# Kernel optimization log

Measured on AMD Instinct MI355X. Metric: run time of the kernel, lower is better.

The kernel has to match this reference:

```python
import jax, jax.numpy as jnp
import numpy as np

B, T, E, H = 8, 2048, 1024, 1024  # batch, seq, embed, head size

def setup_inputs() -> dict:
    key = jax.random.key(0)
    k1, k2, k3, k4 = jax.random.split(key, 4)
    x = jax.random.normal(k1, (B, T, E), dtype=jnp.float32)
    # torch nn.Linear weights are [out, in]; scale down for stability
    Wk = jax.random.normal(k2, (H, E), dtype=jnp.float32) * (E ** -0.5)
    Wq = jax.random.normal(k3, (H, E), dtype=jnp.float32) * (E ** -0.5)
    Wv = jax.random.normal(k4, (H, E), dtype=jnp.float32) * (E ** -0.5)
    return {"x": x, "Wk": Wk, "Wq": Wq, "Wv": Wv}

def reference(x, Wk, Wq, Wv):
    Bx, Tx, Ex = x.shape
    k = jnp.einsum('bte,he->bth', x, Wk)   # [B,T,H]
    q = jnp.einsum('bte,he->bth', x, Wq)
    v = jnp.einsum('bte,he->bth', x, Wv)
    # NOTE: original scales by embed_dim**-0.5 (z = input last dim), not head size
    scores = jnp.einsum('bth,bsh->bts', q, k) * (Ex ** -0.5)  # [B,T,T]
    causal = jnp.tril(jnp.ones((Tx, Tx), dtype=bool))
    scores = jnp.where(causal, scores, -jnp.inf)
    wei = jax.nn.softmax(scores, axis=-1)
    return jnp.einsum('bts,bsh->bth', wei, v)
```

## Files before the change

kernel.cpp:

```cpp
#include <hip/hip_runtime.h>
#include <hip/hip_bf16.h>

typedef unsigned short u16;
typedef __bf16 bf16x8 __attribute__((ext_vector_type(8)));
typedef unsigned short u16x8 __attribute__((ext_vector_type(8)));
typedef unsigned short u16x4 __attribute__((ext_vector_type(4)));
typedef float f32x4 __attribute__((ext_vector_type(4)));
typedef float f32x16 __attribute__((ext_vector_type(16)));

#define B_ 8
#define T_ 2048
#define E_ 1024
#define H_ 1024
#define M_ (B_ * T_)
#define INF __builtin_inff()

__device__ inline u16 f2bf(float f) {
    __bf16 h = (__bf16)f;
    return __builtin_bit_cast(u16, h);
}
__device__ inline float bf2f(u16 u) {
    unsigned v = (unsigned)u << 16;
    return __builtin_bit_cast(float, v);
}
__device__ inline bf16x8 load_frag(const u16* p) {
    u16x8 u = *(const u16x8*)p;
    return __builtin_bit_cast(bf16x8, u);
}
__device__ inline void gload_lds16(const u16* g, u16* l) {
    __builtin_amdgcn_global_load_lds(
        (__attribute__((address_space(1))) unsigned int*)(g),
        (__attribute__((address_space(3))) unsigned int*)(l), 16, 0, 0);
}

__global__ void castk(const float* __restrict__ in, u16* __restrict__ out, int n) {
    int i = (blockIdx.x * blockDim.x + threadIdx.x) * 4;
    if (i < n) {
        f32x4 f = *(const f32x4*)(in + i);
        u16x4 u;
        u[0] = f2bf(f[0]); u[1] = f2bf(f[1]); u[2] = f2bf(f[2]); u[3] = f2bf(f[3]);
        *(u16x4*)(out + i) = u;
    }
}

__global__ __launch_bounds__(256) void gemm_qkv(const u16* __restrict__ A,
                                                const u16* __restrict__ W,
                                                u16* __restrict__ qo,
                                                u16* __restrict__ ko,
                                                u16* __restrict__ vo) {
    const int bm = blockIdx.x, bn = blockIdx.y;
    const int tid = threadIdx.x;
    const int w = tid >> 6, lane = tid & 63, quad = lane >> 4, l16 = lane & 15;
    const int wr = w & 1, wc = w >> 1;

    __shared__ u16 smem[128 * 128];
    u16* As = smem;
    u16* Bs = smem + 128 * 64;

    f32x4 acc[16] = {};

    const u16* Ab = A + (size_t)(bm * 128) * E_;
    const u16* Wb = W + (size_t)(bn * 128) * E_;

    for (int kk = 0; kk < E_; kk += 64) {
        __syncthreads();
#pragma unroll
        for (int i = 0; i < 4; i++) {
            int chunk = i * 256 + tid;
            int row = chunk >> 3, cc = chunk & 7;
            int ccs = cc ^ (row & 7);
            gload_lds16(Ab + (size_t)row * E_ + kk + ccs * 8, &As[chunk * 8]);
            gload_lds16(Wb + (size_t)row * E_ + kk + ccs * 8, &Bs[chunk * 8]);
        }
        __syncthreads();
#pragma unroll
        for (int k2 = 0; k2 < 2; k2++) {
            bf16x8 af[4], bf[4];
#pragma unroll
            for (int ri = 0; ri < 4; ri++) {
                int m = wr * 64 + ri * 16 + l16;
                int slot = m * 8 + ((k2 * 4 + quad) ^ (m & 7));
                af[ri] = load_frag(&As[slot * 8]);
            }
#pragma unroll
            for (int ci = 0; ci < 4; ci++) {
                int n = wc * 64 + ci * 16 + l16;
                int slot = n * 8 + ((k2 * 4 + quad) ^ (n & 7));
                bf[ci] = load_frag(&Bs[slot * 8]);
            }
#pragma unroll
            for (int ri = 0; ri < 4; ri++)
#pragma unroll
                for (int ci = 0; ci < 4; ci++)
                    acc[ri * 4 + ci] = __builtin_amdgcn_mfma_f32_16x16x32_bf16(
                        af[ri], bf[ci], acc[ri * 4 + ci], 0, 0, 0);
        }
    }

    __syncthreads();
    if (bn < 16) {
#pragma unroll
        for (int ri = 0; ri < 4; ri++)
#pragma unroll
            for (int ci = 0; ci < 4; ci++) {
                int n = wc * 64 + ci * 16 + l16;
#pragma unroll
                for (int r = 0; r < 4; r++) {
                    int m = wr * 64 + ri * 16 + quad * 4 + r;
                    smem[m * 128 + (((n >> 3) ^ (m & 15)) << 3) + (n & 7)] =
                        f2bf(acc[ri * 4 + ci][r]);
                }
            }
    } else {
#pragma unroll
        for (int ri = 0; ri < 4; ri++)
#pragma unroll
            for (int ci = 0; ci < 4; ci++) {
                int n = wc * 64 + ci * 16 + l16;
                int m0 = wr * 64 + ri * 16 + quad * 4;
                u16x4 pk;
#pragma unroll
                for (int r = 0; r < 4; r++) pk[r] = f2bf(acc[ri * 4 + ci][r]);
                *(u16x4*)&smem[n * 128 + (((m0 >> 3) ^ (n & 15)) << 3) + (m0 & 7)] = pk;
            }
    }
    __syncthreads();

    const int b = bm >> 4;
    if (bn < 8) {
#pragma unroll
        for (int i = 0; i < 8; i++) {
            int c = i * 256 + tid;
            int m = c >> 4, nc = c & 15;
            u16x8 v = *(u16x8*)&smem[m * 128 + ((nc ^ (m & 15)) << 3)];
            *(u16x8*)&qo[(size_t)(bm * 128 + m) * H_ + bn * 128 + nc * 8] = v;
        }
    } else if (bn < 16) {
#pragma unroll
        for (int i = 0; i < 8; i++) {
            int c = i * 256 + tid;
            int ln = c & 63, h16c = (c >> 6) & 7, s32c = c >> 9;
            int m = s32c * 32 + (ln & 31);
            int nc = h16c * 2 + (ln >> 5);
            u16x8 v = *(u16x8*)&smem[m * 128 + ((nc ^ (m & 15)) << 3)];
            int s32g = (bm & 15) * 4 + s32c;
            int h16g = (bn - 8) * 8 + h16c;
            *(u16x8*)&ko[(((size_t)b * 64 + s32g) * 64 + h16g) * 512 + ln * 8] = v;
        }
    } else {
#pragma unroll
        for (int i = 0; i < 8; i++) {
            int c = i * 256 + tid;
            int ln = c & 63, s16c = (c >> 6) & 7, h32c = c >> 9;
            int n = h32c * 32 + (ln & 31);
            int mc = s16c * 2 + (ln >> 5);
            u16x8 v = *(u16x8*)&smem[n * 128 + ((mc ^ (n & 15)) << 3)];
            int h32g = (bn - 16) * 4 + h32c;
            int s16g = (bm & 15) * 8 + s16c;
            *(u16x8*)&vo[(((size_t)b * 32 + h32g) * 128 + s16g) * 512 + ln * 8] = v;
        }
    }
}

__global__ __launch_bounds__(512, 2) void attn(const u16* __restrict__ qb,
                                               const u16* __restrict__ kfg,
                                               const u16* __restrict__ vfg,
                                               float* __restrict__ out) {
    const int bid = blockIdx.x;
    const int b = bid & 7;
    const int qt = bid >> 3;
    const int t0 = (31 - qt) * 64;
    const int tid = threadIdx.x;
    const int w = tid >> 6, lane = tid & 63;
    const int l5 = lane >> 5, l31 = lane & 31;
    const int srow = tid >> 3, sg = tid & 7;

    __shared__ u16 Qs[64 * 1024];
    __shared__ u16 Sp[2 * 64 * 128];
    float* alphas = (float*)(Sp + 8192);

    const u16* qB = qb + (size_t)b * T_ * H_;
    const u16* kfB = kfg + (size_t)b * 2097152;
    const u16* vfB = vfg + (size_t)b * 2097152;
    const float scale = 0.03125f;

#pragma unroll
    for (int i = 0; i < 16; i++) {
        int s = i * 512 + tid;
        int row = s >> 7, c = s & 127;
        int cc = c ^ (row & 7);
        gload_lds16(qB + (size_t)(t0 + row) * H_ + cc * 8, &Qs[s * 8]);
    }

    float m_r = -INF, l_r = 0.f;
    f32x16 o[2][4] = {};

    const int ct = w & 3;
    const int kh = w >> 2;

    __syncthreads();

    for (int s0 = 0; s0 <= t0 + 63; s0 += 128) {
        const u16* vp = vfB + ((size_t)(w * 4) * 128 + (s0 >> 4)) * 512 + lane * 8;
        bf16x8 vbuf[3][4];
#pragma unroll
        for (int ht = 0; ht < 4; ht++)
            vbuf[0][ht] = load_frag(vp + (size_t)ht * 128 * 512);

        f32x16 sa0 = {}, sa1 = {};
        {
            const u16* kp = kfB + (((size_t)((s0 >> 5) + ct)) * 64 + kh * 32) * 512 + lane * 8;
#pragma unroll 8
            for (int st = 0; st < 32; st++) {
                bf16x8 kf = load_frag(kp + st * 512);
                int cb = (kh * 32 + st) * 2 + l5;
                int x0 = l31 & 7;
                bf16x8 a0 = load_frag(&Qs[((size_t)l31 * 128 + (cb ^ x0)) * 8]);
                bf16x8 a1 = load_frag(&Qs[((size_t)(32 + l31) * 128 + (cb ^ x0)) * 8]);
                __builtin_amdgcn_s_setprio(1);
                sa0 = __builtin_amdgcn_mfma_f32_32x32x16_bf16(a0, kf, sa0, 0, 0, 0);
                sa1 = __builtin_amdgcn_mfma_f32_32x32x16_bf16(a1, kf, sa1, 0, 0, 0);
                __builtin_amdgcn_s_setprio(0);
            }
        }
        __syncthreads();
        {
            u16* Sdst = Sp + kh * 8192;
            int col = ct * 32 + l31;
            int chc = col >> 3, cil = col & 7;
#pragma unroll
            for (int reg = 0; reg < 16; reg++) {
                int row = (reg & 3) + 8 * (reg >> 2) + 4 * l5;
                Sdst[(row * 16 + (chc ^ (row & 7))) * 8 + cil] = f2bf(sa0[reg] * scale);
                int row1 = row + 32;
                Sdst[(row1 * 16 + (chc ^ (row1 & 7))) * 8 + cil] = f2bf(sa1[reg] * scale);
            }
        }
        __syncthreads();

        {
            int sw0 = (sg * 2) ^ (srow & 7), sw1 = (sg * 2 + 1) ^ (srow & 7);
            u16x8 a0 = *(u16x8*)&Sp[(srow * 16 + sw0) * 8];
            u16x8 a1 = *(u16x8*)&Sp[(srow * 16 + sw1) * 8];
            u16x8 b0 = *(u16x8*)&Sp[8192 + (srow * 16 + sw0) * 8];
            u16x8 b1 = *(u16x8*)&Sp[8192 + (srow * 16 + sw1) * 8];
            float v[16];
#pragma unroll
            for (int j = 0; j < 8; j++) v[j] = bf2f(a0[j]) + bf2f(b0[j]);
#pragma unroll
            for (int j = 0; j < 8; j++) v[8 + j] = bf2f(a1[j]) + bf2f(b1[j]);
            int colb = sg * 16;
#pragma unroll
            for (int j = 0; j < 16; j++)
                if (s0 + colb + j > t0 + srow) v[j] = -INF;
            float rmax = v[0];
#pragma unroll
            for (int j = 1; j < 16; j++) rmax = fmaxf(rmax, v[j]);
#pragma unroll
            for (int off = 4; off >= 1; off >>= 1) rmax = fmaxf(rmax, __shfl_xor(rmax, off, 64));
            float mn = fmaxf(m_r, rmax);
            float alpha = __expf(m_r - mn);
            float rsum = 0.f;
            u16x8 p0, p1;
#pragma unroll
            for (int j = 0; j < 8; j++) {
                float p = __expf(v[j] - mn);
                rsum += p; p0[j] = f2bf(p);
            }
#pragma unroll
            for (int j = 0; j < 8; j++) {
                float p = __expf(v[8 + j] - mn);
                rsum += p; p1[j] = f2bf(p);
            }
#pragma unroll
            for (int off = 4; off >= 1; off >>= 1) rsum += __shfl_xor(rsum, off, 64);
            l_r = l_r * alpha + rsum;
            m_r = mn;
            *(u16x8*)&Sp[(srow * 16 + sw0) * 8] = p0;
            *(u16x8*)&Sp[(srow * 16 + sw1) * 8] = p1;
            __syncthreads();
            if (sg == 0) alphas[srow] = alpha;
        }
        __syncthreads();

        {
#pragma unroll
            for (int rg = 0; rg < 2; rg++)
#pragma unroll
                for (int reg = 0; reg < 16; reg++) {
                    float al = alphas[rg * 32 + (reg & 3) + 8 * (reg >> 2) + 4 * l5];
#pragma unroll
                    for (int ht = 0; ht < 4; ht++) o[rg][ht][reg] *= al;
                }
            int xp = l31 & 7;
#pragma unroll
            for (int ht = 0; ht < 4; ht++)
                vbuf[1][ht] = load_frag(vp + ((size_t)ht * 128 + 1) * 512);
#pragma unroll
            for (int sc = 0; sc < 8; sc++) {
                if (sc < 6) {
#pragma unroll
                    for (int ht = 0; ht < 4; ht++)
                        vbuf[(sc + 2) % 3][ht] = load_frag(vp + ((size_t)ht * 128 + sc + 2) * 512);
                }
                bf16x8 p0 = load_frag(&Sp[((size_t)l31 * 16 + ((sc * 2 + l5) ^ xp)) * 8]);
                bf16x8 p1 = load_frag(&Sp[((size_t)(32 + l31) * 16 + ((sc * 2 + l5) ^ xp)) * 8]);
                __builtin_amdgcn_s_setprio(1);
#pragma unroll
                for (int ht = 0; ht < 4; ht++) {
                    o[0][ht] = __builtin_amdgcn_mfma_f32_32x32x16_bf16(p0, vbuf[sc % 3][ht], o[0][ht], 0, 0, 0);
                    o[1][ht] = __builtin_amdgcn_mfma_f32_32x32x16_bf16(p1, vbuf[sc % 3][ht], o[1][ht], 0, 0, 0);
                }
                __builtin_amdgcn_s_setprio(0);
            }
        }
    }

    __syncthreads();
    if (sg == 0) alphas[srow] = l_r;
    __syncthreads();
    float* ob = out + (size_t)b * T_ * H_;
#pragma unroll
    for (int rg = 0; rg < 2; rg++)
#pragma unroll
        for (int reg = 0; reg < 16; reg++) {
            int row = rg * 32 + (reg & 3) + 8 * (reg >> 2) + 4 * l5;
            float linv = 1.f / alphas[row];
#pragma unroll
            for (int ht = 0; ht < 4; ht++) {
                int col = w * 128 + ht * 32 + l31;
                ob[(size_t)(t0 + row) * H_ + col] = o[rg][ht][reg] * linv;
            }
        }
}

extern "C" void kernel_launch(void* const* d_in, const int* in_sizes, int n_in,
                              void* d_out, int out_size, void* d_ws, size_t ws_size,
                              hipStream_t stream) {
    const float* x  = (const float*)d_in[0];
    const float* Wk = (const float*)d_in[1];
    const float* Wq = (const float*)d_in[2];
    const float* Wv = (const float*)d_in[3];
    float* out = (float*)d_out;

    char* ws = (char*)d_ws;
    const size_t SZ_XB  = (size_t)M_ * E_ * 2;
    const size_t SZ_W   = (size_t)3 * H_ * E_ * 2;
    const size_t SZ_QKV = (size_t)M_ * H_ * 2;
    u16* xb   = (u16*)(ws);
    u16* wqkv = (u16*)(ws + SZ_XB);
    u16* qb   = (u16*)(ws + SZ_XB + SZ_W);
    u16* kfb  = (u16*)(ws + SZ_XB + SZ_W + SZ_QKV);
    u16* vfb  = (u16*)(ws + SZ_XB + SZ_W + 2 * SZ_QKV);

    castk<<<M_ * E_ / 4 / 256, 256, 0, stream>>>(x, xb, M_ * E_);
    castk<<<H_ * E_ / 4 / 256, 256, 0, stream>>>(Wq, wqkv, H_ * E_);
    castk<<<H_ * E_ / 4 / 256, 256, 0, stream>>>(Wk, wqkv + (size_t)H_ * E_, H_ * E_);
    castk<<<H_ * E_ / 4 / 256, 256, 0, stream>>>(Wv, wqkv + (size_t)2 * H_ * E_, H_ * E_);

    gemm_qkv<<<dim3(M_ / 128, 3072 / 128), 256, 0, stream>>>(xb, wqkv, qb, kfb, vfb);

    attn<<<dim3(256), 512, 0, stream>>>(qb, kfb, vfb, out);
}
```

Before: 480.7 us.

## Split long causal query tiles across two blocks with a log-sum-exp combine kernel

Query tiles in the second half of the sequence are split into two key ranges (0-1024 and 1024-end), each handled by its own block. Each half writes unnormalized partial outputs plus row max/sum, and a new combine kernel merges them with softmax rescaling. This raises the grid from 256 to 384 blocks to balance the causal workload on the GPU's CUs, and it also prefetches the first 8 K fragments of the next key chunk into registers during the PV phase. The cost is an extra kernel launch, extra global traffic for the partials, and more register pressure. The partials reuse the dead xb workspace region.

```diff
diff --git a/kernel.cpp b/kernel.cpp
--- a/kernel.cpp
+++ b/kernel.cpp
@@ -5,6 +5,7 @@
 typedef __bf16 bf16x8 __attribute__((ext_vector_type(8)));
 typedef unsigned short u16x8 __attribute__((ext_vector_type(8)));
 typedef unsigned short u16x4 __attribute__((ext_vector_type(4)));
+typedef float f32x2 __attribute__((ext_vector_type(2)));
 typedef float f32x4 __attribute__((ext_vector_type(4)));
 typedef float f32x16 __attribute__((ext_vector_type(16)));
 
@@ -165,11 +166,19 @@
 __global__ __launch_bounds__(512, 2) void attn(const u16* __restrict__ qb,
                                                const u16* __restrict__ kfg,
                                                const u16* __restrict__ vfg,
-                                               float* __restrict__ out) {
+                                               float* __restrict__ out,
+                                               float* __restrict__ pout,
+                                               f32x2* __restrict__ mlb) {
     const int bid = blockIdx.x;
     const int b = bid & 7;
-    const int qt = bid >> 3;
-    const int t0 = (31 - qt) * 64;
+    const int u = bid >> 3;
+    int tj, s_begin, mode;
+    if (u < 16)      { tj = 16 + u;  s_begin = 0;    mode = 1; }
+    else if (u < 32) { tj = 31 - u;  s_begin = 0;    mode = 0; }
+    else             { tj = 63 - u;  s_begin = 1024; mode = 2; }
+    const int t0 = tj * 64;
+    const int s_end = (mode == 1) ? 1024 : t0 + 64;
+
     const int tid = threadIdx.x;
     const int w = tid >> 6, lane = tid & 63;
     const int l5 = lane >> 5, l31 = lane & 31;
@@ -183,6 +192,16 @@
     const u16* kfB = kfg + (size_t)b * 2097152;
     const u16* vfB = vfg + (size_t)b * 2097152;
     const float scale = 0.03125f;
+
+    const int ct = w & 3;
+    const int kh = w >> 2;
+
+    bf16x8 kpre[8];
+    {
+        const u16* kp0 = kfB + (((size_t)((s_begin >> 5) + ct)) * 64 + kh * 32) * 512 + lane * 8;
+#pragma unroll
+        for (int i = 0; i < 8; i++) kpre[i] = load_frag(kp0 + i * 512);
+    }
 
 #pragma unroll
     for (int i = 0; i < 16; i++) {
@@ -195,12 +214,9 @@
     float m_r = -INF, l_r = 0.f;
     f32x16 o[2][4] = {};
 
-    const int ct = w & 3;
-    const int kh = w >> 2;
-
     __syncthreads();
 
-    for (int s0 = 0; s0 <= t0 + 63; s0 += 128) {
+    for (int s0 = s_begin; s0 < s_end; s0 += 128) {
         const u16* vp = vfB + ((size_t)(w * 4) * 128 + (s0 >> 4)) * 512 + lane * 8;
         bf16x8 vbuf[3][4];
 #pragma unroll
@@ -210,8 +226,20 @@
         f32x16 sa0 = {}, sa1 = {};
         {
             const u16* kp = kfB + (((size_t)((s0 >> 5) + ct)) * 64 + kh * 32) * 512 + lane * 8;
+#pragma unroll
+            for (int st = 0; st < 8; st++) {
+                bf16x8 kf = kpre[st];
+                int cb = (kh * 32 + st) * 2 + l5;
+                int x0 = l31 & 7;
+                bf16x8 a0 = load_frag(&Qs[((size_t)l31 * 128 + (cb ^ x0)) * 8]);
+                bf16x8 a1 = load_frag(&Qs[((size_t)(32 + l31) * 128 + (cb ^ x0)) * 8]);
+                __builtin_amdgcn_s_setprio(1);
+                sa0 = __builtin_amdgcn_mfma_f32_32x32x16_bf16(a0, kf, sa0, 0, 0, 0);
+                sa1 = __builtin_amdgcn_mfma_f32_32x32x16_bf16(a1, kf, sa1, 0, 0, 0);
+                __builtin_amdgcn_s_setprio(0);
+            }
 #pragma unroll 8
-            for (int st = 0; st < 32; st++) {
+            for (int st = 8; st < 32; st++) {
                 bf16x8 kf = load_frag(kp + st * 512);
                 int cb = (kh * 32 + st) * 2 + l5;
                 int x0 = l31 & 7;
@@ -292,6 +320,11 @@
 #pragma unroll
                     for (int ht = 0; ht < 4; ht++) o[rg][ht][reg] *= al;
                 }
+            if (s0 + 128 < s_end) {
+                const u16* kpn = kfB + (((size_t)(((s0 + 128) >> 5) + ct)) * 64 + kh * 32) * 512 + lane * 8;
+#pragma unroll
+                for (int i = 0; i < 8; i++) kpre[i] = load_frag(kpn + i * 512);
+            }
             int xp = l31 & 7;
 #pragma unroll
             for (int ht = 0; ht < 4; ht++)
@@ -319,19 +352,64 @@
     __syncthreads();
     if (sg == 0) alphas[srow] = l_r;
     __syncthreads();
-    float* ob = out + (size_t)b * T_ * H_;
-#pragma unroll
-    for (int rg = 0; rg < 2; rg++)
-#pragma unroll
-        for (int reg = 0; reg < 16; reg++) {
-            int row = rg * 32 + (reg & 3) + 8 * (reg >> 2) + 4 * l5;
-            float linv = 1.f / alphas[row];
-#pragma unroll
-            for (int ht = 0; ht < 4; ht++) {
-                int col = w * 128 + ht * 32 + l31;
-                ob[(size_t)(t0 + row) * H_ + col] = o[rg][ht][reg] * linv;
-            }
-        }
+    if (mode == 0) {
+        float* ob = out + (size_t)b * T_ * H_;
+#pragma unroll
+        for (int rg = 0; rg < 2; rg++)
+#pragma unroll
+            for (int reg = 0; reg < 16; reg++) {
+                int row = rg * 32 + (reg & 3) + 8 * (reg >> 2) + 4 * l5;
+                float linv = 1.f / alphas[row];
+#pragma unroll
+                for (int ht = 0; ht < 4; ht++) {
+                    int col = w * 128 + ht * 32 + l31;
+                    ob[(size_t)(t0 + row) * H_ + col] = o[rg][ht][reg] * linv;
+                }
+            }
+    } else {
+        if (sg == 0) {
+            f32x2 t; t[0] = m_r; t[1] = l_r;
+            mlb[((size_t)(b * 16 + (tj - 16)) * 2 + (mode - 1)) * 64 + srow] = t;
+        }
+        float* dst = (mode == 1) ? out + ((size_t)b * T_ + t0) * H_
+                                 : pout + (size_t)((b * 16 + (tj - 16)) * 64) * 1024;
+#pragma unroll
+        for (int rg = 0; rg < 2; rg++)
+#pragma unroll
+            for (int reg = 0; reg < 16; reg++) {
+                int row = rg * 32 + (reg & 3) + 8 * (reg >> 2) + 4 * l5;
+#pragma unroll
+                for (int ht = 0; ht < 4; ht++) {
+                    int col = w * 128 + ht * 32 + l31;
+                    dst[(size_t)row * 1024 + col] = o[rg][ht][reg];
+                }
+            }
+    }
+}
+
+__global__ __launch_bounds__(256) void combine(const float* __restrict__ P,
+                                               const f32x2* __restrict__ mlb,
+                                               float* __restrict__ out) {
+    const int bid = blockIdx.x;
+    const int b = bid & 7, jt = (bid >> 3) & 15, rh = bid >> 7;
+    const int t0 = (16 + jt) * 64;
+    const int tcol = threadIdx.x;
+    const float* Pb = P + (size_t)((b * 16 + jt) * 64) * 1024;
+    float* ob = out + ((size_t)b * T_ + t0) * H_;
+    const f32x2* mlA = mlb + (size_t)(b * 16 + jt) * 2 * 64;
+    const f32x2* mlB = mlA + 64;
+#pragma unroll 4
+    for (int r = rh * 32; r < rh * 32 + 32; r++) {
+        f32x2 a = mlA[r], bb = mlB[r];
+        float m = fmaxf(a[0], bb[0]);
+        float wA = __expf(a[0] - m), wB = __expf(bb[0] - m);
+        float denom = a[1] * wA + bb[1] * wB;
+        float cA = wA / denom, cB = wB / denom;
+        f32x4 oa = *(const f32x4*)&ob[(size_t)r * H_ + tcol * 4];
+        f32x4 pv = *(const f32x4*)&Pb[(size_t)r * 1024 + tcol * 4];
+        f32x4 res = oa * cA + pv * cB;
+        *(f32x4*)&ob[(size_t)r * H_ + tcol * 4] = res;
+    }
 }
 
 extern "C" void kernel_launch(void* const* d_in, const int* in_sizes, int n_in,
@@ -352,6 +430,8 @@
     u16* qb   = (u16*)(ws + SZ_XB + SZ_W);
     u16* kfb  = (u16*)(ws + SZ_XB + SZ_W + SZ_QKV);
     u16* vfb  = (u16*)(ws + SZ_XB + SZ_W + 2 * SZ_QKV);
+    float* pout = (float*)ws;
+    f32x2* mlb  = (f32x2*)(ws + SZ_XB);
 
     castk<<<M_ * E_ / 4 / 256, 256, 0, stream>>>(x, xb, M_ * E_);
     castk<<<H_ * E_ / 4 / 256, 256, 0, stream>>>(Wq, wqkv, H_ * E_);
@@ -360,5 +440,6 @@
 
     gemm_qkv<<<dim3(M_ / 128, 3072 / 128), 256, 0, stream>>>(xb, wqkv, qb, kfb, vfb);
 
-    attn<<<dim3(256), 512, 0, stream>>>(qb, kfb, vfb, out);
-}
+    attn<<<dim3(384), 512, 0, stream>>>(qb, kfb, vfb, out, pout, mlb);
+    combine<<<dim3(256), 256, 0, stream>>>(pout, mlb, out);
+}
```

After: 551.9 us. +14.8%, slower.

## Rewrite QKV GEMM with 256x256 tiles, double-buffered LDS and XCD-aware block mapping

Applied to the files above, without the earlier changes.

The QKV projection GEMM moves from 128x128 tiles with 256 threads to 256x256 tiles with 512 threads, raising data reuse per LDS load. It adds double-buffered LDS staging that prefetches the next K tile during MFMA work, with s_setprio and explicit barriers to interleave loads and math. Blocks are remapped over a 1D grid so neighbouring M tiles land on the same XCD for L2 locality. The cost is 128KB of LDS and one block per CU, which lowers occupancy, and only 768 blocks share the CUs.

```diff
diff --git a/kernel.cpp b/kernel.cpp
--- a/kernel.cpp
+++ b/kernel.cpp
@@ -43,120 +43,142 @@
     }
 }
 
-__global__ __launch_bounds__(256) void gemm_qkv(const u16* __restrict__ A,
-                                                const u16* __restrict__ W,
-                                                u16* __restrict__ qo,
-                                                u16* __restrict__ ko,
-                                                u16* __restrict__ vo) {
-    const int bm = blockIdx.x, bn = blockIdx.y;
+__global__ __launch_bounds__(512, 1) void gemm_qkv(const u16* __restrict__ A,
+                                                   const u16* __restrict__ W,
+                                                   u16* __restrict__ qo,
+                                                   u16* __restrict__ ko,
+                                                   u16* __restrict__ vo) {
+    const int id = blockIdx.x;
+    const int xcd = id & 7, rr_ = id >> 3;
+    const int bm = xcd * 8 + (rr_ & 7);
+    const int bn = rr_ >> 3;
     const int tid = threadIdx.x;
     const int w = tid >> 6, lane = tid & 63, quad = lane >> 4, l16 = lane & 15;
-    const int wr = w & 1, wc = w >> 1;
-
-    __shared__ u16 smem[128 * 128];
-    u16* As = smem;
-    u16* Bs = smem + 128 * 64;
-
-    f32x4 acc[16] = {};
-
-    const u16* Ab = A + (size_t)(bm * 128) * E_;
-    const u16* Wb = W + (size_t)(bn * 128) * E_;
-
-    for (int kk = 0; kk < E_; kk += 64) {
+    const int wm = w >> 2, wn = w & 3;
+
+    __shared__ u16 smem[2 * 32768];
+
+    f32x4 acc[8][4] = {};
+
+    const u16* Ab = A + (size_t)(bm * 256) * E_;
+    const u16* Wb = W + (size_t)(bn * 256) * E_;
+
+    auto stage_half = [&](int buf, int mat, int rh, int kt, const u16* gb) {
+#pragma unroll
+        for (int s = 0; s < 2; s++) {
+            int q = s * 512 + tid;
+            int row = rh * 128 + (q >> 3), s8 = q & 7;
+            int c = s8 ^ (row & 7);
+            gload_lds16(gb + (size_t)row * E_ + kt * 64 + c * 8,
+                        &smem[buf * 32768 + mat * 16384 + (row * 8 + s8) * 8]);
+        }
+    };
+
+    stage_half(0, 0, 0, 0, Ab); stage_half(0, 0, 1, 0, Ab);
+    stage_half(0, 1, 0, 0, Wb); stage_half(0, 1, 1, 0, Wb);
+
+    for (int k = 0; k < 16; k++) {
+        const int cur = k & 1;
+        u16* As = &smem[cur * 32768];
+        u16* Bs = &smem[cur * 32768 + 16384];
+
         __syncthreads();
-#pragma unroll
-        for (int i = 0; i < 4; i++) {
-            int chunk = i * 256 + tid;
-            int row = chunk >> 3, cc = chunk & 7;
-            int ccs = cc ^ (row & 7);
-            gload_lds16(Ab + (size_t)row * E_ + kk + ccs * 8, &As[chunk * 8]);
-            gload_lds16(Wb + (size_t)row * E_ + kk + ccs * 8, &Bs[chunk * 8]);
-        }
-        __syncthreads();
-#pragma unroll
-        for (int k2 = 0; k2 < 2; k2++) {
-            bf16x8 af[4], bf[4];
-#pragma unroll
-            for (int ri = 0; ri < 4; ri++) {
-                int m = wr * 64 + ri * 16 + l16;
-                int slot = m * 8 + ((k2 * 4 + quad) ^ (m & 7));
-                af[ri] = load_frag(&As[slot * 8]);
-            }
-#pragma unroll
-            for (int ci = 0; ci < 4; ci++) {
-                int n = wc * 64 + ci * 16 + l16;
-                int slot = n * 8 + ((k2 * 4 + quad) ^ (n & 7));
-                bf[ci] = load_frag(&Bs[slot * 8]);
-            }
-#pragma unroll
-            for (int ri = 0; ri < 4; ri++)
-#pragma unroll
-                for (int ci = 0; ci < 4; ci++)
-                    acc[ri * 4 + ci] = __builtin_amdgcn_mfma_f32_16x16x32_bf16(
-                        af[ri], bf[ci], acc[ri * 4 + ci], 0, 0, 0);
-        }
-    }
-
+
+#pragma unroll
+        for (int p = 0; p < 4; p++) {
+            const int mh = p >> 1, ks = p & 1;
+            bf16x8 af[4], bfr[4];
+#pragma unroll
+            for (int ii = 0; ii < 4; ii++) {
+                int R = wm * 128 + (mh * 4 + ii) * 16 + l16;
+                int c = ks * 4 + quad;
+                af[ii] = load_frag(&As[(R * 8 + (c ^ (R & 7))) * 8]);
+            }
+#pragma unroll
+            for (int jj = 0; jj < 4; jj++) {
+                int R = wn * 64 + jj * 16 + l16;
+                int c = ks * 4 + quad;
+                bfr[jj] = load_frag(&Bs[(R * 8 + (c ^ (R & 7))) * 8]);
+            }
+            if (k < 15 && p < 2) {
+                stage_half(cur ^ 1, p, 0, k + 1, p ? Wb : Ab);
+                stage_half(cur ^ 1, p, 1, k + 1, p ? Wb : Ab);
+            }
+            __builtin_amdgcn_sched_barrier(0);
+            __builtin_amdgcn_s_barrier();
+            asm volatile("s_waitcnt lgkmcnt(0)" ::: "memory");
+            __builtin_amdgcn_sched_barrier(0);
+            __builtin_amdgcn_s_setprio(1);
+#pragma unroll
+            for (int ii = 0; ii < 4; ii++)
+#pragma unroll
+                for (int jj = 0; jj < 4; jj++)
+                    acc[mh * 4 + ii][jj] = __builtin_amdgcn_mfma_f32_16x16x32_bf16(
+                        af[ii], bfr[jj], acc[mh * 4 + ii][jj], 0, 0, 0);
+            __builtin_amdgcn_s_setprio(0);
+            __builtin_amdgcn_s_barrier();
+        }
+    }
+
+    if (bn < 8) {
+#pragma unroll
+        for (int i = 0; i < 8; i++)
+#pragma unroll
+            for (int j = 0; j < 4; j++) {
+                int n = wn * 64 + j * 16 + l16;
+#pragma unroll
+                for (int rg = 0; rg < 4; rg++) {
+                    int m = wm * 128 + i * 16 + quad * 4 + rg;
+                    smem[m * 256 + (((n >> 3) ^ (m & 31)) << 3) + (n & 7)] =
+                        f2bf(acc[i][j][rg]);
+                }
+            }
+    } else {
+#pragma unroll
+        for (int i = 0; i < 8; i++)
+#pragma unroll
+            for (int j = 0; j < 4; j++) {
+                int n = wn * 64 + j * 16 + l16;
+                int m0 = wm * 128 + i * 16 + quad * 4;
+                u16x4 pk;
+#pragma unroll
+                for (int rg = 0; rg < 4; rg++) pk[rg] = f2bf(acc[i][j][rg]);
+                *(u16x4*)&smem[n * 256 + (((m0 >> 3) ^ (n & 31)) << 3) + (m0 & 7)] = pk;
+            }
+    }
     __syncthreads();
-    if (bn < 16) {
-#pragma unroll
-        for (int ri = 0; ri < 4; ri++)
-#pragma unroll
-            for (int ci = 0; ci < 4; ci++) {
-                int n = wc * 64 + ci * 16 + l16;
-#pragma unroll
-                for (int r = 0; r < 4; r++) {
-                    int m = wr * 64 + ri * 16 + quad * 4 + r;
-                    smem[m * 128 + (((n >> 3) ^ (m & 15)) << 3) + (n & 7)] =
-                        f2bf(acc[ri * 4 + ci][r]);
-                }
-            }
-    } else {
-#pragma unroll
-        for (int ri = 0; ri < 4; ri++)
-#pragma unroll
-            for (int ci = 0; ci < 4; ci++) {
-                int n = wc * 64 + ci * 16 + l16;
-                int m0 = wr * 64 + ri * 16 + quad * 4;
-                u16x4 pk;
-#pragma unroll
-                for (int r = 0; r < 4; r++) pk[r] = f2bf(acc[ri * 4 + ci][r]);
-                *(u16x4*)&smem[n * 128 + (((m0 >> 3) ^ (n & 15)) << 3) + (m0 & 7)] = pk;
-            }
-    }
-    __syncthreads();
-
-    const int b = bm >> 4;
-    if (bn < 8) {
-#pragma unroll
-        for (int i = 0; i < 8; i++) {
-            int c = i * 256 + tid;
-            int m = c >> 4, nc = c & 15;
-            u16x8 v = *(u16x8*)&smem[m * 128 + ((nc ^ (m & 15)) << 3)];
-            *(u16x8*)&qo[(size_t)(bm * 128 + m) * H_ + bn * 128 + nc * 8] = v;
-        }
-    } else if (bn < 16) {
-#pragma unroll
-        for (int i = 0; i < 8; i++) {
-            int c = i * 256 + tid;
-            int ln = c & 63, h16c = (c >> 6) & 7, s32c = c >> 9;
+
+    const int b = bm >> 3;
+    if (bn < 4) {
+#pragma unroll
+        for (int i = 0; i < 16; i++) {
+            int c = i * 512 + tid;
+            int m = c >> 5, nc = c & 31;
+            u16x8 v = *(u16x8*)&smem[m * 256 + ((nc ^ (m & 31)) << 3)];
+            *(u16x8*)&qo[(size_t)(bm * 256 + m) * H_ + bn * 256 + nc * 8] = v;
+        }
+    } else if (bn < 8) {
+#pragma unroll
+        for (int i = 0; i < 16; i++) {
+            int c = i * 512 + tid;
+            int ln = c & 63, h16c = (c >> 6) & 15, s32c = c >> 10;
             int m = s32c * 32 + (ln & 31);
             int nc = h16c * 2 + (ln >> 5);
-            u16x8 v = *(u16x8*)&smem[m * 128 + ((nc ^ (m & 15)) << 3)];
-            int s32g = (bm & 15) * 4 + s32c;
-            int h16g = (bn - 8) * 8 + h16c;
+            u16x8 v = *(u16x8*)&smem[m * 256 + ((nc ^ (m & 31)) << 3)];
+            int s32g = (bm & 7) * 8 + s32c;
+            int h16g = (bn - 4) * 16 + h16c;
             *(u16x8*)&ko[(((size_t)b * 64 + s32g) * 64 + h16g) * 512 + ln * 8] = v;
         }
     } else {
 #pragma unroll
-        for (int i = 0; i < 8; i++) {
-            int c = i * 256 + tid;
-            int ln = c & 63, s16c = (c >> 6) & 7, h32c = c >> 9;
+        for (int i = 0; i < 16; i++) {
+            int c = i * 512 + tid;
+            int ln = c & 63, s16c = (c >> 6) & 15, h32c = c >> 10;
             int n = h32c * 32 + (ln & 31);
             int mc = s16c * 2 + (ln >> 5);
-            u16x8 v = *(u16x8*)&smem[n * 128 + ((mc ^ (n & 15)) << 3)];
-            int h32g = (bn - 16) * 4 + h32c;
-            int s16g = (bm & 15) * 8 + s16c;
+            u16x8 v = *(u16x8*)&smem[n * 256 + ((mc ^ (n & 31)) << 3)];
+            int h32g = (bn - 8) * 8 + h32c;
+            int s16g = (bm & 7) * 16 + s16c;
             *(u16x8*)&vo[(((size_t)b * 32 + h32g) * 128 + s16g) * 512 + ln * 8] = v;
         }
     }
@@ -358,7 +380,7 @@
     castk<<<H_ * E_ / 4 / 256, 256, 0, stream>>>(Wk, wqkv + (size_t)H_ * E_, H_ * E_);
     castk<<<H_ * E_ / 4 / 256, 256, 0, stream>>>(Wv, wqkv + (size_t)2 * H_ * E_, H_ * E_);
 
-    gemm_qkv<<<dim3(M_ / 128, 3072 / 128), 256, 0, stream>>>(xb, wqkv, qb, kfb, vfb);
+    gemm_qkv<<<dim3(768), 512, 0, stream>>>(xb, wqkv, qb, kfb, vfb);
 
     attn<<<dim3(256), 512, 0, stream>>>(qb, kfb, vfb, out);
 }
```

New measurement: 455.7 us. 5.2% less time.
